# Kernel optimization log

Measured on AMD Instinct MI355X. Metric: run time of the kernel, lower is better.

## Reference

```python
import jax, jax.numpy as jnp
import numpy as np

B, S, HID = 2, 2048, 2048
NH, NKV, HD = 16, 4, 128
G = NH // NKV  # kv group size
EPS = 1e-6


def setup_inputs() -> dict:
    key = jax.random.key(0)
    ks = jax.random.split(key, 7)
    w = 0.02
    return {
        "hidden_states": jax.random.normal(ks[0], (B, S, HID), dtype=jnp.float32),
        "position_ids": jnp.broadcast_to(jnp.arange(S, dtype=jnp.int64), (B, S)),
        "Wq": jax.random.normal(ks[1], (2 * NH * HD, HID), dtype=jnp.float32) * w,
        "Wk": jax.random.normal(ks[2], (NKV * HD, HID), dtype=jnp.float32) * w,
        "Wv": jax.random.normal(ks[3], (NKV * HD, HID), dtype=jnp.float32) * w,
        "Wo": jax.random.normal(ks[4], (HID, NH * HD), dtype=jnp.float32) * w,
        "norm_w": jnp.zeros((HID,), dtype=jnp.float32),
    }


def reference(hidden_states, position_ids, Wq, Wk, Wv, Wo, norm_w):
    # RMSNorm (weight parameterized as 1 + w, per source)
    ms = jnp.mean(hidden_states * hidden_states, axis=-1, keepdims=True)
    x = hidden_states * jax.lax.rsqrt(ms + EPS) * (1.0 + norm_w)

    qg = x @ Wq.T                                   # (B,S,2*NH*HD)
    q, gate = jnp.split(qg, 2, axis=-1)
    q = q.reshape(B, S, NH, HD).transpose(0, 2, 1, 3)       # (B,NH,S,HD)
    gate = gate.reshape(B, S, NH, HD).transpose(0, 2, 1, 3)
    k = (x @ Wk.T).reshape(B, S, NKV, HD).transpose(0, 2, 1, 3)  # (B,NKV,S,HD)
    v = (x @ Wv.T).reshape(B, S, NKV, HD).transpose(0, 2, 1, 3)

    scale = 1.0 / np.sqrt(HD).astype(np.float32)
    qg4 = q.reshape(B, NKV, G, S, HD)
    attn = jnp.einsum("bkgqd,bkld->bkgql", qg4, k) * scale   # (B,NKV,G,S,S)
    p = jax.nn.softmax(attn, axis=-1)
    o = jnp.einsum("bkgql,bkld->bkgqd", p, v).reshape(B, NH, S, HD)

    o = o * jax.nn.sigmoid(gate)                    # output gate
    o = o.transpose(0, 2, 1, 3).reshape(B, S, NH * HD)
    return o @ Wo.T
```

## Files before the change

### kernel.cpp

```cpp
#include <hip/hip_runtime.h>
#include <math.h>

#define BB    2
#define SS    2048
#define HIDD  2048
#define NHH   16
#define NKVV  4
#define HDD   128
#define MROWS 4096
#define QG_N  4096
#define KV_N  512
#define O_N   2048
#define KDIM  2048
#define EPS_  1e-6f
#define SCALE_ 0.08838834764831845f

typedef __attribute__((ext_vector_type(8))) __bf16 bf16x8;
typedef __attribute__((ext_vector_type(8))) unsigned short u16x8;
typedef __attribute__((ext_vector_type(4))) float f32x4;

__device__ __forceinline__ unsigned short f2bf(float f) {
  return __builtin_bit_cast(unsigned short, (__bf16)f);
}

__global__ __launch_bounds__(256) void f2bf_all(const float* __restrict__ Wq,
                                                const float* __restrict__ Wk,
                                                const float* __restrict__ Wv,
                                                const float* __restrict__ Wo,
                                                unsigned short* __restrict__ dst) {
  const int s0 = QG_N * KDIM / 4;
  const int s1 = s0 + KV_N * KDIM / 4;
  const int s2 = s1 + KV_N * KDIM / 4;
  const int s3 = s2 + O_N * KDIM / 4;
  int i = blockIdx.x * 256 + threadIdx.x;
  if (i >= s3) return;
  float4 v;
  if (i < s0)      v = ((const float4*)Wq)[i];
  else if (i < s1) v = ((const float4*)Wk)[i - s0];
  else if (i < s2) v = ((const float4*)Wv)[i - s1];
  else             v = ((const float4*)Wo)[i - s2];
  ushort4 u;
  u.x = f2bf(v.x); u.y = f2bf(v.y); u.z = f2bf(v.z); u.w = f2bf(v.w);
  ((ushort4*)dst)[i] = u;
}

__global__ __launch_bounds__(256) void rmsnorm_k(const float* __restrict__ h,
                                                 const float* __restrict__ w,
                                                 unsigned short* __restrict__ x) {
  int row = blockIdx.x;
  int t = threadIdx.x;
  const float4* hr = (const float4*)(h + (size_t)row * HIDD);
  const float4* w4 = (const float4*)w;

  float4 v0 = hr[t], v1 = hr[t + 256];
  float ss = v0.x*v0.x + v0.y*v0.y + v0.z*v0.z + v0.w*v0.w
           + v1.x*v1.x + v1.y*v1.y + v1.z*v1.z + v1.w*v1.w;
#pragma unroll
  for (int off = 32; off > 0; off >>= 1) ss += __shfl_down(ss, off, 64);

  __shared__ float part[4];
  __shared__ float rs_sh;
  if ((t & 63) == 0) part[t >> 6] = ss;
  __syncthreads();
  if (t == 0) rs_sh = rsqrtf((part[0]+part[1]+part[2]+part[3]) * (1.0f/HIDD) + EPS_);
  __syncthreads();
  float rs = rs_sh;

  float4 w0 = w4[t], w1 = w4[t + 256];
  ushort4 o0, o1;
  o0.x = f2bf(v0.x * rs * (1.f + w0.x));
  o0.y = f2bf(v0.y * rs * (1.f + w0.y));
  o0.z = f2bf(v0.z * rs * (1.f + w0.z));
  o0.w = f2bf(v0.w * rs * (1.f + w0.w));
  o1.x = f2bf(v1.x * rs * (1.f + w1.x));
  o1.y = f2bf(v1.y * rs * (1.f + w1.y));
  o1.z = f2bf(v1.z * rs * (1.f + w1.z));
  o1.w = f2bf(v1.w * rs * (1.f + w1.w));
  ushort4* xr = (ushort4*)(x + (size_t)row * HIDD);
  xr[t] = o0;
  xr[t + 256] = o1;
}

template <int OBF>
__device__ __forceinline__ void gemm_core(const unsigned short* __restrict__ Ab,
                                          const unsigned short* __restrict__ Bb,
                                          void* __restrict__ Cv,
                                          int Ndim, int bm, int bn,
                                          unsigned short* Als, unsigned short* Bls) {
  char* ldsA = (char*)Als;
  char* ldsB = (char*)Bls;

  int t   = threadIdx.x;
  int r15 = t & 15;
  int g   = (t & 63) >> 4;
  int w   = t >> 6;
  int wr  = w >> 1, wc = w & 1;

  f32x4 acc[4][4] = {};

  for (int k0 = 0; k0 < KDIM; k0 += 64) {
    __syncthreads();
#pragma unroll
    for (int it = 0; it < 4; ++it) {
      int f      = it * 256 + t;
      int row    = f >> 3;
      int schunk = (f & 7) ^ (row & 7);
      unsigned ldsbase = (unsigned)((it * 256 + (w << 6)) << 4);
      __builtin_amdgcn_global_load_lds(
          (const unsigned int*)(Ab + ((size_t)(bm + row) << 11) + k0 + schunk * 8),
          (unsigned int*)(ldsA + ldsbase), 16, 0, 0);
      __builtin_amdgcn_global_load_lds(
          (const unsigned int*)(Bb + ((size_t)(bn + row) << 11) + k0 + schunk * 8),
          (unsigned int*)(ldsB + ldsbase), 16, 0, 0);
    }
    __syncthreads();

#pragma unroll
    for (int tt = 0; tt < 2; ++tt) {
      bf16x8 af[4], bfv[4];
#pragma unroll
      for (int mi = 0; mi < 4; ++mi) {
        int row = wr * 64 + mi * 16 + r15;
        af[mi] = *(const bf16x8*)(ldsA + row * 128 + (((4 * tt + g) ^ (row & 7)) << 4));
      }
#pragma unroll
      for (int ni = 0; ni < 4; ++ni) {
        int row = wc * 64 + ni * 16 + r15;
        bfv[ni] = *(const bf16x8*)(ldsB + row * 128 + (((4 * tt + g) ^ (row & 7)) << 4));
      }
      __builtin_amdgcn_s_setprio(1);
#pragma unroll
      for (int mi = 0; mi < 4; ++mi)
#pragma unroll
        for (int ni = 0; ni < 4; ++ni)
          acc[mi][ni] = __builtin_amdgcn_mfma_f32_16x16x32_bf16(af[mi], bfv[ni], acc[mi][ni], 0, 0, 0);
      __builtin_amdgcn_s_setprio(0);
    }
  }

#pragma unroll
  for (int mi = 0; mi < 4; ++mi)
#pragma unroll
    for (int ni = 0; ni < 4; ++ni) {
      int col = bn + wc * 64 + ni * 16 + r15;
#pragma unroll
      for (int r = 0; r < 4; ++r) {
        int rowg = bm + wr * 64 + mi * 16 + g * 4 + r;
        if (OBF == 1)
          ((unsigned short*)Cv)[(size_t)rowg * Ndim + col] = f2bf(acc[mi][ni][r]);
        else if (OBF == 3) {
          int t6 = rowg & 63;
          int sig = (t6 & 32) + ((t6 & 12) << 1) + ((t6 & 16) >> 2) + (t6 & 3);
          int tokp = (rowg & ~63) | sig;
          ((unsigned short*)Cv)[(size_t)col * MROWS + tokp] = f2bf(acc[mi][ni][r]);
        } else
          ((float*)Cv)[(size_t)rowg * Ndim + col] = acc[mi][ni][r];
      }
    }
}

template <int OBF>
__global__ __launch_bounds__(256) void gemm_bf16(const unsigned short* __restrict__ Ab,
                                                 const unsigned short* __restrict__ Bb,
                                                 void* __restrict__ Cv,
                                                 int Ndim) {
  __shared__ unsigned short Als[128 * 64];
  __shared__ unsigned short Bls[128 * 64];
  gemm_core<OBF>(Ab, Bb, Cv, Ndim, blockIdx.y * 128, blockIdx.x * 128, Als, Bls);
}

__global__ __launch_bounds__(256) void gemm_kv(const unsigned short* __restrict__ Ab,
                                               const unsigned short* __restrict__ Wk,
                                               const unsigned short* __restrict__ Wv,
                                               unsigned short* __restrict__ Ck,
                                               unsigned short* __restrict__ Cvt) {
  __shared__ unsigned short Als[128 * 64];
  __shared__ unsigned short Bls[128 * 64];
  int bx = blockIdx.x;
  if (bx < 4)
    gemm_core<1>(Ab, Wk, (void*)Ck, KV_N, blockIdx.y * 128, bx * 128, Als, Bls);
  else
    gemm_core<3>(Ab, Wv, (void*)Cvt, KV_N, blockIdx.y * 128, (bx & 3) * 128, Als, Bls);
}

#define LD8(basep, r, x) \
  (*(const bf16x8*)((basep) + (size_t)(r) * 128 + ((((x) ^ ((r)&7))) << 4)))

#define STAGE_A(bufi, h, tk)                                                   \
  { _Pragma("unroll")                                                          \
    for (int c = 0; c < 2; ++c) {                                              \
      int f = c * 512 + t;                                                     \
      int rr = f >> 3;                                                         \
      int sc = (f & 7) ^ (rr & 7);                                             \
      __builtin_amdgcn_global_load_lds(                                        \
        (const unsigned int*)(Ab + ((size_t)(bm + (h)*128 + rr) << 11) + (tk)*64 + sc*8), \
        (unsigned int*)(lds8 + (bufi)*32768 + (h)*16384 + c*8192 + (w<<10)), 16, 0, 0); \
    } }

#define STAGE_B(bufi, h, tk)                                                   \
  { _Pragma("unroll")                                                          \
    for (int c = 0; c < 2; ++c) {                                              \
      int f = c * 512 + t;                                                     \
      int rr = f >> 3;                                                         \
      int sc = (f & 7) ^ (rr & 7);                                             \
      __builtin_amdgcn_global_load_lds(                                        \
        (const unsigned int*)(Bbp + ((size_t)(bn + (h)*128 + rr) << 11) + (tk)*64 + sc*8), \
        (unsigned int*)(lds8 + 65536 + (bufi)*32768 + (h)*16384 + c*8192 + (w<<10)), 16, 0, 0); \
    } }

#define RD_A(SRC, MIBASE)                                                      \
  { _Pragma("unroll")                                                          \
    for (int mi = 0; mi < 4; ++mi) {                                           \
      int rr = wr * 128 + ((MIBASE) + mi) * 16 + r15;                          \
      afr[mi][0] = LD8(SRC, rr, g);                                            \
      afr[mi][1] = LD8(SRC, rr, 4 + g);                                        \
    } }

#define RD_B(SRC, NIBASE, DST)                                                 \
  { _Pragma("unroll")                                                          \
    for (int ni = 0; ni < 2; ++ni) {                                           \
      int rr = wc * 64 + ((NIBASE) + ni) * 16 + r15;                           \
      DST[ni][0] = LD8(SRC, rr, g);                                            \
      DST[ni][1] = LD8(SRC, rr, 4 + g);                                        \
    } }

#define MFMA_QUAD(MIBASE, NIBASE, BREG)                                        \
  { __builtin_amdgcn_s_setprio(1);                                             \
    _Pragma("unroll")                                                          \
    for (int mi = 0; mi < 4; ++mi)                                             \
      _Pragma("unroll")                                                        \
      for (int ni = 0; ni < 2; ++ni)                                           \
        _Pragma("unroll")                                                      \
        for (int ks = 0; ks < 2; ++ks)                                         \
          acc[(MIBASE)+mi][(NIBASE)+ni] =                                      \
            __builtin_amdgcn_mfma_f32_16x16x32_bf16(afr[mi][ks], BREG[ni][ks], \
                                                    acc[(MIBASE)+mi][(NIBASE)+ni], 0, 0, 0); \
    __builtin_amdgcn_s_setprio(0); }

#define BAR() __builtin_amdgcn_s_barrier()

__global__ __launch_bounds__(512, 2) void gemm_qg256(const unsigned short* __restrict__ Ab,
                                                     const unsigned short* __restrict__ Bbp,
                                                     unsigned short* __restrict__ Cq,
                                                     float* __restrict__ Cg) {
  __shared__ char lds8[131072];
  int t = threadIdx.x;
  int r15 = t & 15, g = (t & 63) >> 4, w = t >> 6;
  int wr = w >> 2, wc = w & 3;
  int bm = blockIdx.y * 256, bn = blockIdx.x * 256;
  char* A0 = lds8;            char* A1 = lds8 + 32768;
  char* B0 = lds8 + 65536;    char* B1 = lds8 + 98304;

  f32x4 acc[8][4] = {};
  bf16x8 afr[4][2], b0r[2][2], b1r[2][2];

  STAGE_A(0, 0, 0); STAGE_A(0, 1, 0); STAGE_B(0, 0, 0); STAGE_B(0, 1, 0);
  STAGE_A(1, 0, 1); STAGE_A(1, 1, 1); STAGE_B(1, 0, 1); STAGE_B(1, 1, 1);
  asm volatile("s_waitcnt vmcnt(8)" ::: "memory");
  BAR();

  for (int i = 0; i < 15; ++i) {
    int te = 2 * i + 2, to = 2 * i + 3;
    RD_A(A0, 0); RD_B(B0, 0, b0r);
    BAR(); MFMA_QUAD(0, 0, b0r); BAR();
    RD_B(B0, 2, b1r);
    BAR(); MFMA_QUAD(0, 2, b1r); BAR();
    RD_A(A0, 4);
    STAGE_B(0, 0, te);
    BAR(); MFMA_QUAD(4, 0, b0r); BAR();
    STAGE_A(0, 0, te);
    BAR(); MFMA_QUAD(4, 2, b1r);
    asm volatile("s_waitcnt vmcnt(4)" ::: "memory");
    BAR();
    RD_A(A1, 0); RD_B(B1, 0, b0r);
    STAGE_A(0, 1, te);
    BAR(); MFMA_QUAD(0, 0, b0r); BAR();
    RD_B(B1, 2, b1r);
    STAGE_B(0, 1, te);
    BAR(); MFMA_QUAD(0, 2, b1r); BAR();
    RD_A(A1, 4);
    STAGE_B(1, 0, to); STAGE_B(1, 1, to);
    BAR(); MFMA_QUAD(4, 0, b0r); BAR();
    STAGE_A(1, 0, to); STAGE_A(1, 1, to);
    BAR(); MFMA_QUAD(4, 2, b1r);
    asm volatile("s_waitcnt vmcnt(8)" ::: "memory");
    BAR();
  }
  RD_A(A0, 0); RD_B(B0, 0, b0r);
  BAR(); MFMA_QUAD(0, 0, b0r); BAR();
  RD_B(B0, 2, b1r);
  BAR(); MFMA_QUAD(0, 2, b1r); BAR();
  RD_A(A0, 4);
  BAR(); MFMA_QUAD(4, 0, b0r); BAR();
  BAR(); MFMA_QUAD(4, 2, b1r);
  asm volatile("s_waitcnt vmcnt(0)" ::: "memory");
  BAR();
  RD_A(A1, 0); RD_B(B1, 0, b0r);
  BAR(); MFMA_QUAD(0, 0, b0r); BAR();
  RD_B(B1, 2, b1r);
  BAR(); MFMA_QUAD(0, 2, b1r); BAR();
  RD_A(A1, 4);
  BAR(); MFMA_QUAD(4, 0, b0r); BAR();
  BAR(); MFMA_QUAD(4, 2, b1r);

  bool isq = (bn < O_N);
  int colbase = bn + wc * 64;
#pragma unroll
  for (int mi = 0; mi < 8; ++mi) {
    size_t row = (size_t)bm + wr * 128 + mi * 16 + g * 4;
#pragma unroll
    for (int ni = 0; ni < 4; ++ni) {
      int col = colbase + ni * 16 + r15;
#pragma unroll
      for (int r = 0; r < 4; ++r) {
        if (isq) Cq[(row + r) * O_N + col] = f2bf(acc[mi][ni][r] * SCALE_);
        else     Cg[(row + r) * O_N + (col - O_N)] = acc[mi][ni][r];
      }
    }
  }
}

#define OST_A(bufi, h, tk)                                                     \
  { _Pragma("unroll")                                                          \
    for (int c = 0; c < 2; ++c) {                                              \
      int f = c * 512 + t;                                                     \
      int rr = f >> 3;                                                         \
      int sc = (f & 7) ^ (rr & 7);                                             \
      __builtin_amdgcn_global_load_lds(                                        \
        (const unsigned int*)(Ab + ((size_t)(bm + (h)*128 + rr) << 11) + (tk)*64 + sc*8), \
        (unsigned int*)(lds8 + (bufi)*32768 + (h)*16384 + c*8192 + (w<<10)), 16, 0, 0); \
    } }

#define OST_B(bufi, tk)                                                        \
  { _Pragma("unroll")                                                          \
    for (int c = 0; c < 2; ++c) {                                              \
      int f = c * 512 + t;                                                     \
      int rr = f >> 3;                                                         \
      int sc = (f & 7) ^ (rr & 7);                                             \
      __builtin_amdgcn_global_load_lds(                                        \
        (const unsigned int*)(Bbp + ((size_t)(bn + rr) << 11) + (tk)*64 + sc*8), \
        (unsigned int*)(lds8 + 65536 + (bufi)*16384 + c*8192 + (w<<10)), 16, 0, 0); \
    } }

#define ORD_A(bufi)                                                            \
  { const char* abase = lds8 + (bufi)*32768 + (wr >> 1)*16384;                 \
    _Pragma("unroll")                                                          \
    for (int mi = 0; mi < 4; ++mi) {                                           \
      int rl = ((wr & 1) * 64) + mi * 16 + r15;                                \
      afr[mi][0] = LD8(abase, rl, g);                                          \
      afr[mi][1] = LD8(abase, rl, 4 + g);                                      \
    } }

#define ORD_B(bufi, NIBASE, DST)                                               \
  { const char* bbase = lds8 + 65536 + (bufi)*16384;                           \
    _Pragma("unroll")                                                          \
    for (int ni = 0; ni < 2; ++ni) {                                           \
      int rl = wc * 64 + ((NIBASE) + ni) * 16 + r15;                           \
      DST[ni][0] = LD8(bbase, rl, g);                                          \
      DST[ni][1] = LD8(bbase, rl, 4 + g);                                      \
    } }

#define OMFMA(NIBASE, BREG)                                                    \
  { __builtin_amdgcn_s_setprio(1);                                             \
    _Pragma("unroll")                                                          \
    for (int mi = 0; mi < 4; ++mi)                                             \
      _Pragma("unroll")                                                        \
      for (int ni = 0; ni < 2; ++ni)                                           \
        _Pragma("unroll")                                                      \
        for (int ks = 0; ks < 2; ++ks)                                         \
          acc[mi][(NIBASE)+ni] =                                               \
            __builtin_amdgcn_mfma_f32_16x16x32_bf16(afr[mi][ks], BREG[ni][ks], \
                                                    acc[mi][(NIBASE)+ni], 0, 0, 0); \
    __builtin_amdgcn_s_setprio(0); }

__global__ __launch_bounds__(512, 2) void gemm_o256(const unsigned short* __restrict__ Ab,
                                                    const unsigned short* __restrict__ Bbp,
                                                    float* __restrict__ C) {
  __shared__ char lds8[98304];
  int t = threadIdx.x;
  int r15 = t & 15, g = (t & 63) >> 4, w = t >> 6;
  int wr = w >> 1, wc = w & 1;
  int bm = blockIdx.y * 256, bn = blockIdx.x * 128;

  f32x4 acc[4][4] = {};
  bf16x8 afr[4][2], b0r[2][2], b1r[2][2];

  OST_A(0, 0, 0); OST_A(0, 1, 0); OST_B(0, 0);
  OST_A(1, 0, 1); OST_A(1, 1, 1);
  asm volatile("s_waitcnt vmcnt(4)" ::: "memory");
  BAR();

  for (int i = 0; i < 15; ++i) {
    int to = 2 * i + 1, te2 = 2 * i + 2, to2 = 2 * i + 3;
    ORD_A(0); ORD_B(0, 0, b0r);
    OST_B(1, to);
    BAR(); OMFMA(0, b0r); BAR();
    ORD_B(0, 2, b1r);
    OST_A(0, 0, te2);
    BAR(); OMFMA(2, b1r);
    asm volatile("s_waitcnt vmcnt(2)" ::: "memory");
    BAR();
    ORD_A(1); ORD_B(1, 0, b0r);
    OST_A(0, 1, te2); OST_B(0, te2);
    BAR(); OMFMA(0, b0r); BAR();
    ORD_B(1, 2, b1r);
    OST_A(1, 0, to2); OST_A(1, 1, to2);
    BAR(); OMFMA(2, b1r);
    asm volatile("s_waitcnt vmcnt(4)" ::: "memory");
    BAR();
  }
  ORD_A(0); ORD_B(0, 0, b0r);
  OST_B(1, 31);
  BAR(); OMFMA(0, b0r); BAR();
  ORD_B(0, 2, b1r);
  BAR(); OMFMA(2, b1r);
  asm volatile("s_waitcnt vmcnt(0)" ::: "memory");
  BAR();
  ORD_A(1); ORD_B(1, 0, b0r);
  BAR(); OMFMA(0, b0r); BAR();
  ORD_B(1, 2, b1r);
  BAR(); OMFMA(2, b1r);

#pragma unroll
  for (int mi = 0; mi < 4; ++mi) {
    size_t row = (size_t)bm + wr * 64 + mi * 16 + g * 4;
#pragma unroll
    for (int ni = 0; ni < 4; ++ni) {
      int col = bn + wc * 64 + ni * 16 + r15;
#pragma unroll
      for (int r = 0; r < 4; ++r)
        C[(row + r) * O_N + col] = acc[mi][ni][r];
    }
  }
}

__global__ __launch_bounds__(256, 2) void attn_mfma(const unsigned short* __restrict__ qb,
                                                    const float* __restrict__ gateb,
                                                    const unsigned short* __restrict__ kb,
                                                    const unsigned short* __restrict__ vt,
                                                    unsigned short* __restrict__ obuf) {
  __shared__ unsigned short Ks[2][64 * 128];
  __shared__ unsigned short Vt[2][128 * 64];
  char* ldsK0 = (char*)Ks;
  char* ldsV0 = (char*)Vt;

  int t = threadIdx.x;
  int l = t & 63, w = t >> 6;
  int c15 = l & 15, g = l >> 4;
  int bid = blockIdx.x;
  int swz = (bid & 7) * 64 + (bid >> 3);
  int qt = swz & 15, h = (swz >> 4) & 15, b = swz >> 8;
  int kh = h >> 2;
  size_t rowQ0 = (size_t)b * SS + (size_t)qt * 128;
  size_t rowKbase = (size_t)b * SS;

  bf16x8 qf[2][4];
#pragma unroll
  for (int qi = 0; qi < 2; ++qi)
#pragma unroll
    for (int ks = 0; ks < 4; ++ks)
      qf[qi][ks] = *(const bf16x8*)(qb + (rowQ0 + w * 32 + qi * 16 + c15) * O_N
                                       + h * HDD + g * 8 + ks * 32);

  f32x4 accO[2][8] = {};
  float mrun[2] = {-INFINITY, -INFINITY};
  float lrun[2] = {0.f, 0.f};

#define ISSUE_K(bufi, kt_)                                                     \
  {                                                                            \
    size_t rowK0 = rowKbase + (size_t)(kt_) * 64;                              \
    _Pragma("unroll")                                                          \
    for (int it = 0; it < 4; ++it) {                                           \
      int f = it * 256 + t;                                                    \
      int kv = f >> 4;                                                         \
      int schunk = (f & 15) ^ (kv & 7);                                        \
      unsigned ldsbase = (unsigned)((it * 256 + (w << 6)) << 4);               \
      __builtin_amdgcn_global_load_lds(                                        \
          (const unsigned int*)(kb + (rowK0 + kv) * KV_N + kh * HDD + schunk * 8), \
          (unsigned int*)(ldsK0 + (bufi) * 16384 + ldsbase), 16, 0, 0);        \
    }                                                                          \
  }
#define ISSUE_VT(bufi, kt_)                                                    \
  {                                                                            \
    size_t tokbase = rowKbase + (size_t)(kt_) * 64;                            \
    _Pragma("unroll")                                                          \
    for (int it = 0; it < 4; ++it) {                                           \
      int f = it * 256 + t;                                                    \
      int row = f >> 3;                                                        \
      int schunk = (f & 7) ^ (row & 7);                                        \
      unsigned ldsbase = (unsigned)((it * 256 + (w << 6)) << 4);               \
      __builtin_amdgcn_global_load_lds(                                        \
          (const unsigned int*)(vt + (size_t)(kh * 128 + row) * MROWS + tokbase + schunk * 8), \
          (unsigned int*)(ldsV0 + (bufi) * 16384 + ldsbase), 16, 0, 0);        \
    }                                                                          \
  }

  ISSUE_K(0, 0);
  ISSUE_VT(0, 0);
  asm volatile("s_waitcnt vmcnt(0)" ::: "memory");
  __syncthreads();

  const int NT = SS / 64;
  for (int kt = 0; kt < NT; ++kt) {
    int cur = kt & 1, nxt = cur ^ 1;
    char* ldsK = ldsK0 + cur * 16384;
    char* ldsV = ldsV0 + cur * 16384;

    if (kt + 1 < NT) {
      ISSUE_K(nxt, kt + 1);
      ISSUE_VT(nxt, kt + 1);
    }

    f32x4 accS[2][4] = {};
    __builtin_amdgcn_s_setprio(1);
#pragma unroll
    for (int nf = 0; nf < 4; ++nf) {
      int kvr = nf * 16 + c15;
#pragma unroll
      for (int ks = 0; ks < 4; ++ks) {
        bf16x8 kf = *(const bf16x8*)(ldsK + kvr * 256 + ((((g + 4 * ks) ^ (kvr & 7)) << 4)));
#pragma unroll
        for (int qi = 0; qi < 2; ++qi)
          accS[qi][nf] = __builtin_amdgcn_mfma_f32_16x16x32_bf16(kf, qf[qi][ks], accS[qi][nf], 0, 0, 0);
      }
    }
    __builtin_amdgcn_s_setprio(0);

    float mt[2];
#pragma unroll
    for (int qi = 0; qi < 2; ++qi) {
      float m0 = fmaxf(fmaxf(accS[qi][0][0], accS[qi][0][1]), fmaxf(accS[qi][0][2], accS[qi][0][3]));
#pragma unroll
      for (int nf = 1; nf < 4; ++nf)
        m0 = fmaxf(m0, fmaxf(fmaxf(accS[qi][nf][0], accS[qi][nf][1]), fmaxf(accS[qi][nf][2], accS[qi][nf][3])));
      m0 = fmaxf(m0, __shfl_xor(m0, 16, 64));
      m0 = fmaxf(m0, __shfl_xor(m0, 32, 64));
      mt[qi] = m0;
    }

    bool safe = (mt[0] <= mrun[0] + 8.f) && (mt[1] <= mrun[1] + 8.f);
    if (!__all(safe)) {
#pragma unroll
      for (int qi = 0; qi < 2; ++qi) {
        float mnew = fmaxf(mrun[qi], mt[qi]);
        float al = __expf(mrun[qi] - mnew);
        mrun[qi] = mnew;
        lrun[qi] *= al;
        float alr[4];
#pragma unroll
        for (int r = 0; r < 4; ++r) alr[r] = __shfl(al, g * 4 + r, 16);
#pragma unroll
        for (int df = 0; df < 8; ++df)
#pragma unroll
          for (int r = 0; r < 4; ++r) accO[qi][df][r] *= alr[r];
      }
    }

    u16x8 pfr[2][2];
#pragma unroll
    for (int qi = 0; qi < 2; ++qi) {
      float ps = 0.f;
#pragma unroll
      for (int nf = 0; nf < 4; ++nf) {
        float p0 = __expf(accS[qi][nf][0] - mrun[qi]);
        float p1 = __expf(accS[qi][nf][1] - mrun[qi]);
        float p2 = __expf(accS[qi][nf][2] - mrun[qi]);
        float p3 = __expf(accS[qi][nf][3] - mrun[qi]);
        ps += (p0 + p1) + (p2 + p3);
        pfr[qi][nf >> 1][(nf & 1) * 4 + 0] = f2bf(p0);
        pfr[qi][nf >> 1][(nf & 1) * 4 + 1] = f2bf(p1);
        pfr[qi][nf >> 1][(nf & 1) * 4 + 2] = f2bf(p2);
        pfr[qi][nf >> 1][(nf & 1) * 4 + 3] = f2bf(p3);
      }
      ps += __shfl_xor(ps, 16, 64);
      ps += __shfl_xor(ps, 32, 64);
      lrun[qi] += ps;
    }

    __builtin_amdgcn_s_setprio(1);
#pragma unroll
    for (int ks2 = 0; ks2 < 2; ++ks2) {
      bf16x8 pf0 = __builtin_bit_cast(bf16x8, pfr[0][ks2]);
      bf16x8 pf1 = __builtin_bit_cast(bf16x8, pfr[1][ks2]);
#pragma unroll
      for (int df = 0; df < 8; ++df) {
        int d = df * 16 + c15;
        bf16x8 vf = *(const bf16x8*)(ldsV + d * 128 + ((((g + 4 * ks2) ^ (d & 7)) << 4)));
        accO[0][df] = __builtin_amdgcn_mfma_f32_16x16x32_bf16(pf0, vf, accO[0][df], 0, 0, 0);
        accO[1][df] = __builtin_amdgcn_mfma_f32_16x16x32_bf16(pf1, vf, accO[1][df], 0, 0, 0);
      }
    }
    __builtin_amdgcn_s_setprio(0);

    if (kt + 1 < NT) {
      asm volatile("s_waitcnt vmcnt(0)" ::: "memory");
    }
    __syncthreads();
  }

#pragma unroll
  for (int qi = 0; qi < 2; ++qi) {
    float invL = 1.f / lrun[qi];
    float ivr[4];
#pragma unroll
    for (int r = 0; r < 4; ++r) ivr[r] = __shfl(invL, g * 4 + r, 16);
#pragma unroll
    for (int r = 0; r < 4; ++r) {
      size_t row = rowQ0 + w * 32 + qi * 16 + g * 4 + r;
#pragma unroll
      for (int df = 0; df < 8; ++df) {
        int d = df * 16 + c15;
        float gt = gateb[row * (size_t)O_N + h * HDD + d];
        float sg = 1.f / (1.f + __expf(-gt));
        obuf[row * (size_t)O_N + h * HDD + d] = f2bf(accO[qi][df][r] * ivr[r] * sg);
      }
    }
  }
#undef ISSUE_K
#undef ISSUE_VT
}

extern "C" void kernel_launch(void* const* d_in, const int* in_sizes, int n_in,
                              void* d_out, int out_size, void* d_ws, size_t ws_size,
                              hipStream_t stream) {
  const float* hs = (const float*)d_in[0];
  const float* Wq = (const float*)d_in[2];
  const float* Wk = (const float*)d_in[3];
  const float* Wv = (const float*)d_in[4];
  const float* Wo = (const float*)d_in[5];
  const float* nw = (const float*)d_in[6];
  float* out = (float*)d_out;

  float* gateb = (float*)d_ws;
  unsigned short* qb16 = (unsigned short*)(gateb + (size_t)MROWS * O_N);
  unsigned short* kb16 = qb16 + (size_t)MROWS * O_N;
  unsigned short* vt16 = kb16 + (size_t)MROWS * KV_N;
  unsigned short* xb   = vt16 + (size_t)KV_N * MROWS;
  unsigned short* ob   = xb   + (size_t)MROWS * HIDD;
  unsigned short* wqb  = ob   + (size_t)MROWS * O_N;
  unsigned short* wkb  = wqb  + (size_t)QG_N * KDIM;
  unsigned short* wvb  = wkb  + (size_t)KV_N * KDIM;
  unsigned short* wob  = wvb  + (size_t)KV_N * KDIM;

  const int tot4 = (QG_N + KV_N + KV_N + O_N) * KDIM / 4;
  f2bf_all<<<(tot4 + 255) / 256, 256, 0, stream>>>(Wq, Wk, Wv, Wo, wqb);
  rmsnorm_k<<<MROWS, 256, 0, stream>>>(hs, nw, xb);

  gemm_qg256<<<dim3(QG_N/256, MROWS/256), 512, 0, stream>>>(xb, wqb, qb16, gateb);
  gemm_kv<<<dim3(8, MROWS/128), 256, 0, stream>>>(xb, wkb, wvb, kb16, vt16);
  attn_mfma<<<dim3(512), 256, 0, stream>>>(qb16, gateb, kb16, vt16, ob);
  gemm_o256<<<dim3(O_N/128, MROWS/256), 512, 0, stream>>>(ob, wob, out);
}
```

Before: 250.7 us.

## Load V fragments directly to registers, use exp2 softmax, defer row-sum reduction

Drops the V LDS staging buffer and loads each wave's V^T fragments straight from global memory into registers at the start of every KV tile. The log2(e) factor is folded into the Q scaling so the softmax can use exp2f, with the rescale threshold adjusted to match. Per-lane partial row sums are now kept and reduced across lanes only once at the end. This cuts LDS traffic and per-tile shuffles, but adds register pressure, and every wave fetches V redundantly from global memory with less latency hiding than the old double-buffered prefetch.

```diff
diff --git a/kernel.cpp b/kernel.cpp
--- a/kernel.cpp
+++ b/kernel.cpp
@@ -14,6 +14,8 @@
 #define KDIM  2048
 #define EPS_  1e-6f
 #define SCALE_ 0.08838834764831845f
+#define SCALE2_ (0.08838834764831845f * 1.4426950408889634f)
+#define THR2_  11.5417f
 
 typedef __attribute__((ext_vector_type(8))) __bf16 bf16x8;
 typedef __attribute__((ext_vector_type(8))) unsigned short u16x8;
@@ -313,7 +315,7 @@
       int col = colbase + ni * 16 + r15;
 #pragma unroll
       for (int r = 0; r < 4; ++r) {
-        if (isq) Cq[(row + r) * O_N + col] = f2bf(acc[mi][ni][r] * SCALE_);
+        if (isq) Cq[(row + r) * O_N + col] = f2bf(acc[mi][ni][r] * SCALE2_);
         else     Cg[(row + r) * O_N + (col - O_N)] = acc[mi][ni][r];
       }
     }
@@ -440,9 +442,7 @@
                                                     const unsigned short* __restrict__ vt,
                                                     unsigned short* __restrict__ obuf) {
   __shared__ unsigned short Ks[2][64 * 128];
-  __shared__ unsigned short Vt[2][128 * 64];
   char* ldsK0 = (char*)Ks;
-  char* ldsV0 = (char*)Vt;
 
   int t = threadIdx.x;
   int l = t & 63, w = t >> 6;
@@ -465,6 +465,7 @@
   f32x4 accO[2][8] = {};
   float mrun[2] = {-INFINITY, -INFINITY};
   float lrun[2] = {0.f, 0.f};
+  u16x8 vreg[2][8];
 
 #define ISSUE_K(bufi, kt_)                                                     \
   {                                                                            \
@@ -480,23 +481,20 @@
           (unsigned int*)(ldsK0 + (bufi) * 16384 + ldsbase), 16, 0, 0);        \
     }                                                                          \
   }
-#define ISSUE_VT(bufi, kt_)                                                    \
+#define LOAD_V(kt_)                                                            \
   {                                                                            \
     size_t tokbase = rowKbase + (size_t)(kt_) * 64;                            \
     _Pragma("unroll")                                                          \
-    for (int it = 0; it < 4; ++it) {                                           \
-      int f = it * 256 + t;                                                    \
-      int row = f >> 3;                                                        \
-      int schunk = (f & 7) ^ (row & 7);                                        \
-      unsigned ldsbase = (unsigned)((it * 256 + (w << 6)) << 4);               \
-      __builtin_amdgcn_global_load_lds(                                        \
-          (const unsigned int*)(vt + (size_t)(kh * 128 + row) * MROWS + tokbase + schunk * 8), \
-          (unsigned int*)(ldsV0 + (bufi) * 16384 + ldsbase), 16, 0, 0);        \
-    }                                                                          \
+    for (int ks2 = 0; ks2 < 2; ++ks2)                                          \
+      _Pragma("unroll")                                                        \
+      for (int df = 0; df < 8; ++df) {                                         \
+        int d = df * 16 + c15;                                                 \
+        vreg[ks2][df] = *(const u16x8*)(vt + (size_t)(kh * 128 + d) * MROWS    \
+                                           + tokbase + 32 * ks2 + 8 * g);      \
+      }                                                                        \
   }
 
   ISSUE_K(0, 0);
-  ISSUE_VT(0, 0);
   asm volatile("s_waitcnt vmcnt(0)" ::: "memory");
   __syncthreads();
 
@@ -504,12 +502,9 @@
   for (int kt = 0; kt < NT; ++kt) {
     int cur = kt & 1, nxt = cur ^ 1;
     char* ldsK = ldsK0 + cur * 16384;
-    char* ldsV = ldsV0 + cur * 16384;
-
-    if (kt + 1 < NT) {
-      ISSUE_K(nxt, kt + 1);
-      ISSUE_VT(nxt, kt + 1);
-    }
+
+    LOAD_V(kt);
+    if (kt + 1 < NT) ISSUE_K(nxt, kt + 1);
 
     f32x4 accS[2][4] = {};
     __builtin_amdgcn_s_setprio(1);
@@ -538,12 +533,12 @@
       mt[qi] = m0;
     }
 
-    bool safe = (mt[0] <= mrun[0] + 8.f) && (mt[1] <= mrun[1] + 8.f);
+    bool safe = (mt[0] <= mrun[0] + THR2_) && (mt[1] <= mrun[1] + THR2_);
     if (!__all(safe)) {
 #pragma unroll
       for (int qi = 0; qi < 2; ++qi) {
         float mnew = fmaxf(mrun[qi], mt[qi]);
-        float al = __expf(mrun[qi] - mnew);
+        float al = exp2f(mrun[qi] - mnew);
         mrun[qi] = mnew;
         lrun[qi] *= al;
         float alr[4];
@@ -562,18 +557,16 @@
       float ps = 0.f;
 #pragma unroll
       for (int nf = 0; nf < 4; ++nf) {
-        float p0 = __expf(accS[qi][nf][0] - mrun[qi]);
-        float p1 = __expf(accS[qi][nf][1] - mrun[qi]);
-        float p2 = __expf(accS[qi][nf][2] - mrun[qi]);
-        float p3 = __expf(accS[qi][nf][3] - mrun[qi]);
+        float p0 = exp2f(accS[qi][nf][0] - mrun[qi]);
+        float p1 = exp2f(accS[qi][nf][1] - mrun[qi]);
+        float p2 = exp2f(accS[qi][nf][2] - mrun[qi]);
+        float p3 = exp2f(accS[qi][nf][3] - mrun[qi]);
         ps += (p0 + p1) + (p2 + p3);
         pfr[qi][nf >> 1][(nf & 1) * 4 + 0] = f2bf(p0);
         pfr[qi][nf >> 1][(nf & 1) * 4 + 1] = f2bf(p1);
         pfr[qi][nf >> 1][(nf & 1) * 4 + 2] = f2bf(p2);
         pfr[qi][nf >> 1][(nf & 1) * 4 + 3] = f2bf(p3);
       }
-      ps += __shfl_xor(ps, 16, 64);
-      ps += __shfl_xor(ps, 32, 64);
       lrun[qi] += ps;
     }
 
@@ -584,8 +577,7 @@
       bf16x8 pf1 = __builtin_bit_cast(bf16x8, pfr[1][ks2]);
 #pragma unroll
       for (int df = 0; df < 8; ++df) {
-        int d = df * 16 + c15;
-        bf16x8 vf = *(const bf16x8*)(ldsV + d * 128 + ((((g + 4 * ks2) ^ (d & 7)) << 4)));
+        bf16x8 vf = __builtin_bit_cast(bf16x8, vreg[ks2][df]);
         accO[0][df] = __builtin_amdgcn_mfma_f32_16x16x32_bf16(pf0, vf, accO[0][df], 0, 0, 0);
         accO[1][df] = __builtin_amdgcn_mfma_f32_16x16x32_bf16(pf1, vf, accO[1][df], 0, 0, 0);
       }
@@ -600,6 +592,8 @@
 
 #pragma unroll
   for (int qi = 0; qi < 2; ++qi) {
+    lrun[qi] += __shfl_xor(lrun[qi], 16, 64);
+    lrun[qi] += __shfl_xor(lrun[qi], 32, 64);
     float invL = 1.f / lrun[qi];
     float ivr[4];
 #pragma unroll
@@ -617,7 +611,7 @@
     }
   }
 #undef ISSUE_K
-#undef ISSUE_VT
+#undef LOAD_V
 }
 
 extern "C" void kernel_launch(void* const* d_in, const int* in_sizes, int n_in,
```

After: 312.4 us. 24.6% more time.
